# Kernel tuning notes

Hardware: AMD Instinct MI355X
Metric: run time of the kernel (lower is better)

The kernel has to match this reference:

```python
import jax, jax.numpy as jnp
import numpy as np

B, S, D, H, F = 8, 1024, 1024, 16, 4096
DH = D // H  # 64
EPS = 1e-12


def _layer_norm(x, g, b):
    mu = jnp.mean(x, axis=-1, keepdims=True)
    var = jnp.mean(jnp.square(x - mu), axis=-1, keepdims=True)
    return (x - mu) / jnp.sqrt(var + EPS) * g + b


def setup_inputs() -> dict:
    key = jax.random.key(0)
    ks = jax.random.split(key, 16)
    sd = 0.02
    inp = {
        "x": jax.random.normal(ks[0], (B, S, D), dtype=jnp.float32),
        "attn_mask": jnp.ones((B, S), dtype=jnp.int32),
        # attention projections (torch Linear: W is [out, in])
        "Wq": jax.random.normal(ks[1], (D, D), dtype=jnp.float32) * sd,
        "bq": jnp.zeros((D,), dtype=jnp.float32),
        "Wk": jax.random.normal(ks[2], (D, D), dtype=jnp.float32) * sd,
        "bk": jnp.zeros((D,), dtype=jnp.float32),
        "Wv": jax.random.normal(ks[3], (D, D), dtype=jnp.float32) * sd,
        "bv": jnp.zeros((D,), dtype=jnp.float32),
        "Wo": jax.random.normal(ks[4], (D, D), dtype=jnp.float32) * sd,
        "bo": jnp.zeros((D,), dtype=jnp.float32),
        # sa_layer_norm
        "ln1_g": jnp.ones((D,), dtype=jnp.float32),
        "ln1_b": jnp.zeros((D,), dtype=jnp.float32),
        # FFN
        "W1": jax.random.normal(ks[5], (F, D), dtype=jnp.float32) * sd,
        "b1": jnp.zeros((F,), dtype=jnp.float32),
        "W2": jax.random.normal(ks[6], (D, F), dtype=jnp.float32) * sd,
        "b2": jnp.zeros((D,), dtype=jnp.float32),
        # output_layer_norm
        "ln2_g": jnp.ones((D,), dtype=jnp.float32),
        "ln2_b": jnp.zeros((D,), dtype=jnp.float32),
    }
    return inp


def reference(x, attn_mask, Wq, bq, Wk, bk, Wv, bv, Wo, bo,
              ln1_g, ln1_b, W1, b1, W2, b2, ln2_g, ln2_b):
    b, s, d = x.shape

    def proj_heads(inp, W, bias):
        y = jnp.einsum('bsd,ed->bse', inp, W) + bias  # torch Linear: x @ W.T + b
        return y.reshape(b, s, H, DH).transpose(0, 2, 1, 3)  # (b, h, s, dh)

    q = proj_heads(x, Wq, bq) / jnp.sqrt(jnp.float32(DH))
    k = proj_heads(x, Wk, bk)
    v = proj_heads(x, Wv, bv)

    scores = jnp.einsum('bhqe,bhke->bhqk', q, k)  # (b, h, s, s)
    pad = (attn_mask == 0)[:, None, None, :]      # (b, 1, 1, s)
    scores = jnp.where(pad, -jnp.inf, scores)
    weights = jax.nn.softmax(scores, axis=-1)

    ctx = jnp.einsum('bhqk,bhke->bhqe', weights, v)
    ctx = ctx.transpose(0, 2, 1, 3).reshape(b, s, d)
    sa_out = jnp.einsum('bsd,ed->bse', ctx, Wo) + bo

    h = _layer_norm(sa_out + x, ln1_g, ln1_b)

    ff = jnp.einsum('bsd,fd->bsf', h, W1) + b1
    ff = jax.nn.gelu(ff, approximate=False)
    ff = jnp.einsum('bsf,df->bsd', ff, W2) + b2

    out = _layer_norm(ff + h, ln2_g, ln2_b)
    return out
```

## Files before the change

### kernel.cpp

```cpp
#include <hip/hip_runtime.h>
#include <math.h>

typedef __attribute__((ext_vector_type(8))) short short8;
typedef __attribute__((ext_vector_type(4))) float f32x4;

__device__ __forceinline__ unsigned short f2bf(float f) {
  unsigned int u = __float_as_uint(f);
  u += 0x7fffu + ((u >> 16) & 1u);
  return (unsigned short)(u >> 16);
}

__device__ __forceinline__ float gelu_f(float v) {
  float xa = fabsf(v) * 0.70710678118f;
  float t = __builtin_amdgcn_rcpf(1.f + 0.3275911f * xa);
  float p = t * (0.254829592f +
            t * (-0.284496736f +
            t * (1.421413741f +
            t * (-1.453152027f + t * 1.061405429f))));
  float erfa = 1.f - p * __expf(-xa * xa);
  return 0.5f * v * (1.f + copysignf(erfa, v));
}

__device__ __forceinline__ void gll16(const unsigned short* g, unsigned short* l) {
  __builtin_amdgcn_global_load_lds(
      (const __attribute__((address_space(1))) unsigned int*)(uintptr_t)g,
      (__attribute__((address_space(3))) unsigned int*)(uintptr_t)l, 16, 0, 0);
}

__global__ __launch_bounds__(256) void cvt_all(
    const float* __restrict__ Wq, const float* __restrict__ Wk,
    const float* __restrict__ Wv, const float* __restrict__ Wo,
    const float* __restrict__ W1, const float* __restrict__ W2,
    const float* __restrict__ x, unsigned short* __restrict__ ws) {
  const int bi = blockIdx.x;
  const float* in;
  unsigned short* out;
  int i;
  if (bi < 4096) {
    const int m = bi >> 10;
    in = (m == 0) ? Wq : (m == 1) ? Wk : (m == 2) ? Wv : Wo;
    out = ws + (size_t)m * (1u << 20);
    i = (bi & 1023) * 256 + threadIdx.x;
  } else if (bi < 8192) {
    in = W1; out = ws + (4u << 20); i = (bi - 4096) * 256 + threadIdx.x;
  } else if (bi < 12288) {
    in = W2; out = ws + (8u << 20); i = (bi - 8192) * 256 + threadIdx.x;
  } else {
    in = x; out = ws + (12u << 20); i = (bi - 12288) * 256 + threadIdx.x;
  }
  float4 f = reinterpret_cast<const float4*>(in)[i];
  ushort4 o;
  o.x = f2bf(f.x); o.y = f2bf(f.y); o.z = f2bf(f.z); o.w = f2bf(f.w);
  reinterpret_cast<ushort4*>(out)[i] = o;
}

#define MFMA_SUB(f0, SA)                                                      \
  {                                                                           \
    __builtin_amdgcn_s_setprio(1);                                            \
    _Pragma("unroll") for (int fi = 0; fi < 2; ++fi) {                        \
      _Pragma("unroll") for (int j = 0; j < NREP; ++j) {                      \
        if constexpr (SWAP) {                                                 \
          acc[(f0) + fi][j] = __builtin_amdgcn_mfma_f32_16x16x32_bf16(        \
              bf[j][0], SA[fi][0], acc[(f0) + fi][j], 0, 0, 0);               \
        } else {                                                              \
          acc[(f0) + fi][j] = __builtin_amdgcn_mfma_f32_16x16x32_bf16(        \
              SA[fi][0], bf[j][0], acc[(f0) + fi][j], 0, 0, 0);               \
        }                                                                     \
      }                                                                       \
    }                                                                         \
    _Pragma("unroll") for (int fi = 0; fi < 2; ++fi) {                        \
      _Pragma("unroll") for (int j = 0; j < NREP; ++j) {                      \
        if constexpr (SWAP) {                                                 \
          acc[(f0) + fi][j] = __builtin_amdgcn_mfma_f32_16x16x32_bf16(        \
              bf[j][1], SA[fi][1], acc[(f0) + fi][j], 0, 0, 0);               \
        } else {                                                              \
          acc[(f0) + fi][j] = __builtin_amdgcn_mfma_f32_16x16x32_bf16(        \
              SA[fi][1], bf[j][1], acc[(f0) + fi][j], 0, 0, 0);               \
        }                                                                     \
      }                                                                       \
    }                                                                         \
    __builtin_amdgcn_s_setprio(0);                                            \
  }

#define READ_AF(SET, f0)                                                      \
  {                                                                           \
    SET[0][0] = *reinterpret_cast<const short8*>(                             \
        &Asc[abase + ((f0) * 16) * 64 + s0]);                                 \
    SET[0][1] = *reinterpret_cast<const short8*>(                             \
        &Asc[abase + ((f0) * 16) * 64 + s1]);                                 \
    SET[1][0] = *reinterpret_cast<const short8*>(                             \
        &Asc[abase + ((f0) * 16 + 16) * 64 + s0]);                            \
    SET[1][1] = *reinterpret_cast<const short8*>(                             \
        &Asc[abase + ((f0) * 16 + 16) * 64 + s1]);                            \
  }

#define READ_BF                                                               \
  _Pragma("unroll") for (int j = 0; j < NREP; ++j) {                          \
    bf[j][0] = *reinterpret_cast<const short8*>(                              \
        &Bsc[bbase + (j * 16) * 64 + s0]);                                    \
    bf[j][1] = *reinterpret_cast<const short8*>(                              \
        &Bsc[bbase + (j * 16) * 64 + s1]);                                    \
  }

#define LGKM(n)                                                               \
  asm volatile("s_waitcnt lgkmcnt(" #n ")" ::: "memory");                     \
  __builtin_amdgcn_sched_barrier(0)

#define MEMFENCE asm volatile("" ::: "memory")
#define BAR __builtin_amdgcn_s_barrier()

template <int EPI, int BN, bool SWAP>
__global__ __launch_bounds__(512, 2) void gemm_big(
    const unsigned short* __restrict__ A, const unsigned short* __restrict__ B,
    const float* __restrict__ bias, const float* __restrict__ bias_k,
    int K, int N, const float* __restrict__ resid,
    unsigned short* __restrict__ outb, float* __restrict__ outf) {
  constexpr int WN = BN / 4;
  constexpr int NREP = WN / 16;
  constexpr int BGRP = BN / 64;
  __shared__ __align__(16) unsigned short As[2][256 * 64];
  __shared__ __align__(16) unsigned short Bs[2][BN * 64];

  const int t = threadIdx.x;
  const int lane = t & 63, wv = t >> 6;
  const int wm = wv >> 2, wn = wv & 3;
  const int l15 = lane & 15, quad = lane >> 4;

  const int gx = gridDim.x;
  const int nwg = gx * gridDim.y;
  int lin = blockIdx.y * gx + blockIdx.x;
  lin = (lin & 7) * (nwg >> 3) + (lin >> 3);
  const int gxs = 31 - __clz(gx);
  const int tn = (lin & (gx - 1)) * BN;
  const int tm = (lin >> gxs) * 256;

  const int srow = lane >> 3;
  const int scol = ((lane & 7) ^ srow) << 3;
  const unsigned short* pA[4];
  const unsigned short* pB[BGRP];
#pragma unroll
  for (int g = 0; g < 4; ++g)
    pA[g] = &A[(size_t)(tm + g * 64 + wv * 8 + srow) * K + scol];
#pragma unroll
  for (int g = 0; g < BGRP; ++g)
    pB[g] = &B[(size_t)(tn + g * 64 + wv * 8 + srow) * K + scol];

  const int abase = (wm * 128 + l15) * 64;
  const int bbase = (wn * WN + l15) * 64;
  const int s0 = ((quad ^ (l15 & 7)) << 3);
  const int s1 = (((quad + 4) ^ (l15 & 7)) << 3);

  const f32x4 zero = {0.f, 0.f, 0.f, 0.f};
  f32x4 acc[8][NREP];
#pragma unroll
  for (int i = 0; i < 8; ++i)
#pragma unroll
    for (int j = 0; j < NREP; ++j) acc[i][j] = zero;
  short8 afA[2][2], afB[2][2], bf[NREP][2];

#pragma unroll
  for (int g = 0; g < 4; ++g) {
    gll16(pA[g], &As[0][(g * 64 + wv * 8) * 64]);
    pA[g] += 64;
  }
#pragma unroll
  for (int g = 0; g < BGRP; ++g) {
    gll16(pB[g], &Bs[0][(g * 64 + wv * 8) * 64]);
    pB[g] += 64;
  }
  asm volatile("s_waitcnt vmcnt(0)" ::: "memory");
  BAR;
  MEMFENCE;

  const int NT = K >> 6;
  for (int tt = 0; tt < NT; ++tt) {
    const unsigned short* Asc = As[tt & 1];
    const unsigned short* Bsc = Bs[tt & 1];
    unsigned short* Asn = As[(tt + 1) & 1];
    unsigned short* Bsn = Bs[(tt + 1) & 1];

    if (tt + 1 < NT) {
#pragma unroll
      for (int g = 0; g < 4; ++g) {
        gll16(pA[g], &Asn[(g * 64 + wv * 8) * 64]);
        pA[g] += 64;
      }
#pragma unroll
      for (int g = 0; g < BGRP; ++g) {
        gll16(pB[g], &Bsn[(g * 64 + wv * 8) * 64]);
        pB[g] += 64;
      }
    }

    READ_BF;
    READ_AF(afA, 0);
    READ_AF(afB, 2);
    LGKM(4);
    MFMA_SUB(0, afA);
    READ_AF(afA, 4);
    LGKM(4);
    MFMA_SUB(2, afB);
    READ_AF(afB, 6);
    LGKM(4);
    MFMA_SUB(4, afA);
    LGKM(0);
    MFMA_SUB(6, afB);

    if (tt + 1 < NT) {
      asm volatile("s_waitcnt vmcnt(0)" ::: "memory");
      BAR;
      MEMFENCE;
    }
  }

  if constexpr (!SWAP) {
    const int rb2 = tm + wm * 128 + (quad << 2);
    const int cb2 = tn + wn * WN + l15;
#pragma unroll
    for (int i = 0; i < 8; ++i) {
      const int row0 = rb2 + i * 16;
#pragma unroll
      for (int j = 0; j < NREP; ++j) {
        const int col = cb2 + j * 16;
        const float bcol = bias[col];
        const int h = col >> 6, dh = col & 63;
        const int b = row0 >> 10, s0r = row0 & 1023;
        ushort4 pk;
        pk.x = f2bf(acc[i][j][0] + bcol);
        pk.y = f2bf(acc[i][j][1] + bcol);
        pk.z = f2bf(acc[i][j][2] + bcol);
        pk.w = f2bf(acc[i][j][3] + bcol);
        *reinterpret_cast<ushort4*>(
            &outb[(((size_t)((b << 4) + h)) << 16) + (dh << 10) + s0r]) = pk;
      }
    }
  } else {
    const int rb = tm + wm * 128 + l15;
    const int cb = tn + wn * WN + (quad << 2);
#pragma unroll
    for (int i = 0; i < 8; ++i) {
      const int row = rb + i * 16;
#pragma unroll
      for (int j = 0; j < NREP; ++j) {
        const int col0 = cb + j * 16;
        if constexpr (EPI == 5) {
          const int chunk = col0 >> 10;
          const int colc = col0 & 1023;
          const float4 b4 = *reinterpret_cast<const float4*>(
              &(chunk == 0 ? bias : bias_k)[colc]);
          const float sc = (chunk == 0) ? 0.125f : 1.f;
          const int h = colc >> 6, dh = colc & 63;
          const int b = row >> 10, s = row & 1023;
          ushort4 pk;
          pk.x = f2bf((acc[i][j][0] + b4.x) * sc);
          pk.y = f2bf((acc[i][j][1] + b4.y) * sc);
          pk.z = f2bf((acc[i][j][2] + b4.z) * sc);
          pk.w = f2bf((acc[i][j][3] + b4.w) * sc);
          *reinterpret_cast<ushort4*>(
              &outb[((size_t)chunk << 23) + (((size_t)((b << 4) + h)) << 16) +
                    (s << 6) + dh]) = pk;
        } else if constexpr (EPI == 2) {
          const float4 b4 = *reinterpret_cast<const float4*>(&bias[col0]);
          ushort4 pk;
          pk.x = f2bf(gelu_f(acc[i][j][0] + b4.x));
          pk.y = f2bf(gelu_f(acc[i][j][1] + b4.y));
          pk.z = f2bf(gelu_f(acc[i][j][2] + b4.z));
          pk.w = f2bf(gelu_f(acc[i][j][3] + b4.w));
          *reinterpret_cast<ushort4*>(&outb[(size_t)row * (size_t)N + col0]) = pk;
        } else {
          const float4 b4 = *reinterpret_cast<const float4*>(&bias[col0]);
          const size_t idx = (size_t)row * (size_t)N + col0;
          const float4 r4 = *reinterpret_cast<const float4*>(&resid[idx]);
          float4 o4;
          o4.x = acc[i][j][0] + b4.x + r4.x;
          o4.y = acc[i][j][1] + b4.y + r4.y;
          o4.z = acc[i][j][2] + b4.z + r4.z;
          o4.w = acc[i][j][3] + b4.w + r4.w;
          *reinterpret_cast<float4*>(&outf[idx]) = o4;
        }
      }
    }
  }
}
#undef MFMA_SUB
#undef READ_AF
#undef READ_BF
#undef LGKM
#undef MEMFENCE
#undef BAR

__global__ __launch_bounds__(256) void attn_kernel(
    const unsigned short* __restrict__ Q, const unsigned short* __restrict__ Kc,
    const unsigned short* __restrict__ Vg, const int* __restrict__ mask,
    unsigned short* __restrict__ ctx) {
  __shared__ __align__(16) unsigned short Ks[2][64 * 64];
  __shared__ __align__(16) unsigned short Vs[2][64 * 64];
  __shared__ __align__(16) unsigned short Ps[4][16 * 72];
  __shared__ float maskf[1024];
  const int t = threadIdx.x;
  const int bh = blockIdx.x;
  const int qt = blockIdx.y;
  const int b = bh >> 4, h = bh & 15;
  const int lane = t & 63, wv = t >> 6, l15 = lane & 15, quad = lane >> 4;
  const int lr = lane >> 3;
  const int cs = (lane & 7) ^ lr;
  const unsigned short* Qp = Q + ((size_t)bh << 16);
  const unsigned short* Kp = Kc + ((size_t)bh << 16);
  const unsigned short* Vp = Vg + ((size_t)bh << 16);
  const int seg0 = wv * 2, seg1 = wv * 2 + 1;
  const int r0 = seg0 * 8 + lr, r1 = seg1 * 8 + lr;

  for (int i = t; i < 1024; i += 256)
    maskf[i] = mask[b * 1024 + i] ? -8.f : -INFINITY;

  short8 qf[2][2];
#pragma unroll
  for (int g = 0; g < 2; ++g)
#pragma unroll
    for (int hh = 0; hh < 2; ++hh)
      qf[g][hh] = *reinterpret_cast<const short8*>(
          &Qp[(size_t)(qt * 128 + wv * 32 + g * 16 + l15) * 64 + hh * 32 + quad * 8]);

  gll16(&Kp[r0 * 64 + cs * 8], &Ks[0][seg0 * 512]);
  gll16(&Kp[r1 * 64 + cs * 8], &Ks[0][seg1 * 512]);
  gll16(&Vp[r0 * 1024 + cs * 8], &Vs[0][seg0 * 512]);
  gll16(&Vp[r1 * 1024 + cs * 8], &Vs[0][seg1 * 512]);

  const int sw0 = ((quad ^ (l15 & 7)) << 3);
  const int sw1 = (((quad + 4) ^ (l15 & 7)) << 3);
  const f32x4 zero = {0.f, 0.f, 0.f, 0.f};
  float ps[2][4];
  f32x4 o[2][4];
#pragma unroll
  for (int g = 0; g < 2; ++g)
#pragma unroll
    for (int j = 0; j < 4; ++j) { o[g][j] = zero; ps[g][j] = 0.f; }

  unsigned short* Pw = Ps[wv];
  for (int kt = 0; kt < 16; ++kt) {
    __syncthreads();
    const int cur = kt & 1;
    if (kt < 15) {
      const int nb = cur ^ 1;
      gll16(&Kp[((kt + 1) * 64 + r0) * 64 + cs * 8], &Ks[nb][seg0 * 512]);
      gll16(&Kp[((kt + 1) * 64 + r1) * 64 + cs * 8], &Ks[nb][seg1 * 512]);
      gll16(&Vp[r0 * 1024 + (kt + 1) * 64 + cs * 8], &Vs[nb][seg0 * 512]);
      gll16(&Vp[r1 * 1024 + (kt + 1) * 64 + cs * 8], &Vs[nb][seg1 * 512]);
    }
    float madd[4];
    short8 kf[4][2];
#pragma unroll
    for (int nt = 0; nt < 4; ++nt) {
      const int row = (nt * 16 + l15) * 64;
      kf[nt][0] = *reinterpret_cast<const short8*>(&Ks[cur][row + sw0]);
      kf[nt][1] = *reinterpret_cast<const short8*>(&Ks[cur][row + sw1]);
      madd[nt] = maskf[kt * 64 + nt * 16 + l15];
    }
#pragma unroll
    for (int g = 0; g < 2; ++g) {
      f32x4 s4[4];
#pragma unroll
      for (int nt = 0; nt < 4; ++nt)
        s4[nt] = __builtin_amdgcn_mfma_f32_16x16x32_bf16(qf[g][0], kf[nt][0], zero, 0, 0, 0);
#pragma unroll
      for (int nt = 0; nt < 4; ++nt)
        s4[nt] = __builtin_amdgcn_mfma_f32_16x16x32_bf16(qf[g][1], kf[nt][1], s4[nt], 0, 0, 0);
#pragma unroll
      for (int nt = 0; nt < 4; ++nt) {
#pragma unroll
        for (int r = 0; r < 4; ++r) {
          float p = __expf(s4[nt][r] + madd[nt]);
          ps[g][r] += p;
          Pw[(quad * 4 + r) * 72 + nt * 16 + l15] = f2bf(p);
        }
      }
      short8 pf0 = *reinterpret_cast<const short8*>(&Pw[l15 * 72 + quad * 8]);
      short8 pf1 = *reinterpret_cast<const short8*>(&Pw[l15 * 72 + 32 + quad * 8]);
      short8 vf[4][2];
#pragma unroll
      for (int nt = 0; nt < 4; ++nt) {
        const int row = (nt * 16 + l15) * 64;
        vf[nt][0] = *reinterpret_cast<const short8*>(&Vs[cur][row + sw0]);
        vf[nt][1] = *reinterpret_cast<const short8*>(&Vs[cur][row + sw1]);
      }
#pragma unroll
      for (int nt = 0; nt < 4; ++nt)
        o[g][nt] = __builtin_amdgcn_mfma_f32_16x16x32_bf16(pf0, vf[nt][0], o[g][nt], 0, 0, 0);
#pragma unroll
      for (int nt = 0; nt < 4; ++nt)
        o[g][nt] = __builtin_amdgcn_mfma_f32_16x16x32_bf16(pf1, vf[nt][1], o[g][nt], 0, 0, 0);
    }
  }

#pragma unroll
  for (int g = 0; g < 2; ++g)
#pragma unroll
    for (int r = 0; r < 4; ++r) {
      float v = ps[g][r];
#pragma unroll
      for (int off = 8; off >= 1; off >>= 1) v += __shfl_xor(v, off, 64);
      const float inv = 1.f / v;
      const int srow = qt * 128 + wv * 32 + g * 16 + quad * 4 + r;
#pragma unroll
      for (int nt = 0; nt < 4; ++nt) {
        const int dh = nt * 16 + l15;
        ctx[((size_t)b << 20) + ((size_t)srow << 10) + (h << 6) + dh] =
            f2bf(o[g][nt][r] * inv);
      }
    }
}

__global__ __launch_bounds__(256) void ln_kernel(float* __restrict__ y,
                                                 const float* __restrict__ g,
                                                 const float* __restrict__ be,
                                                 unsigned short* __restrict__ hb) {
  __shared__ float sm[8];
  const int t = threadIdx.x;
  const size_t row = blockIdx.x;
  float* yr = y + (row << 10);
  float v[4];
#pragma unroll
  for (int i = 0; i < 4; ++i) v[i] = yr[t + (i << 8)];
  float s = v[0] + v[1] + v[2] + v[3];
#pragma unroll
  for (int off = 32; off >= 1; off >>= 1) s += __shfl_xor(s, off, 64);
  if ((t & 63) == 0) sm[t >> 6] = s;
  __syncthreads();
  float mu = (sm[0] + sm[1] + sm[2] + sm[3]) * (1.f / 1024.f);
  float q = 0.f;
#pragma unroll
  for (int i = 0; i < 4; ++i) { float d = v[i] - mu; q += d * d; }
#pragma unroll
  for (int off = 32; off >= 1; off >>= 1) q += __shfl_xor(q, off, 64);
  if ((t & 63) == 0) sm[4 + (t >> 6)] = q;
  __syncthreads();
  float var = (sm[4] + sm[5] + sm[6] + sm[7]) * (1.f / 1024.f);
  float rs = rsqrtf(var + 1e-12f);
#pragma unroll
  for (int i = 0; i < 4; ++i) {
    int c = t + (i << 8);
    float o = (v[i] - mu) * rs * g[c] + be[c];
    yr[c] = o;
    if (hb) hb[(row << 10) + c] = f2bf(o);
  }
}

extern "C" void kernel_launch(void* const* d_in, const int* in_sizes, int n_in,
                              void* d_out, int out_size, void* d_ws, size_t ws_size,
                              hipStream_t stream) {
  const float* x   = (const float*)d_in[0];
  const int*   msk = (const int*)d_in[1];
  const float* Wq  = (const float*)d_in[2];
  const float* bq  = (const float*)d_in[3];
  const float* Wk  = (const float*)d_in[4];
  const float* bk  = (const float*)d_in[5];
  const float* Wv  = (const float*)d_in[6];
  const float* bv  = (const float*)d_in[7];
  const float* Wo  = (const float*)d_in[8];
  const float* bo  = (const float*)d_in[9];
  const float* g1  = (const float*)d_in[10];
  const float* be1 = (const float*)d_in[11];
  const float* W1  = (const float*)d_in[12];
  const float* b1  = (const float*)d_in[13];
  const float* W2  = (const float*)d_in[14];
  const float* b2  = (const float*)d_in[15];
  const float* g2  = (const float*)d_in[16];
  const float* be2 = (const float*)d_in[17];
  float* out = (float*)d_out;

  unsigned short* Wqb = (unsigned short*)d_ws;
  unsigned short* Wvb = Wqb + (2u << 20);
  unsigned short* Wob = Wvb + (1u << 20);
  unsigned short* W1b = Wob + (1u << 20);
  unsigned short* W2b = W1b + (4u << 20);
  unsigned short* xb  = W2b + (4u << 20);
  unsigned short* qb  = xb + (8u << 20);
  unsigned short* vb  = qb + (16u << 20);
  unsigned short* ctx = xb;
  unsigned short* ffb = xb;
  float* y1 = (float*)(qb + (24u << 20));
  unsigned short* hb = (unsigned short*)(y1 + (8u << 20));

  dim3 blk(256), blk5(512);
  cvt_all<<<dim3(20480), blk, 0, stream>>>(Wq, Wk, Wv, Wo, W1, W2, x, (unsigned short*)d_ws);
  gemm_big<5, 256, true><<<dim3(8, 32), blk5, 0, stream>>>(xb, Wqb, bq, bk, 1024, 2048,
                                                           nullptr, qb, nullptr);
  gemm_big<4, 128, false><<<dim3(8, 32), blk5, 0, stream>>>(xb, Wvb, bv, nullptr, 1024, 1024,
                                                            nullptr, vb, nullptr);
  attn_kernel<<<dim3(128, 8), blk, 0, stream>>>(qb, qb + (8u << 20), vb, msk, ctx);
  gemm_big<1, 128, true><<<dim3(8, 32), blk5, 0, stream>>>(ctx, Wob, bo, nullptr, 1024, 1024,
                                                           x, nullptr, y1);
  ln_kernel<<<dim3(8192), blk, 0, stream>>>(y1, g1, be1, hb);
  gemm_big<2, 256, true><<<dim3(16, 32), blk5, 0, stream>>>(hb, W1b, b1, nullptr, 1024, 4096,
                                                            nullptr, ffb, nullptr);
  gemm_big<1, 128, true><<<dim3(8, 32), blk5, 0, stream>>>(ffb, W2b, b2, nullptr, 4096, 1024,
                                                           y1, nullptr, out);
  ln_kernel<<<dim3(8192), blk, 0, stream>>>(out, g2, be2, nullptr);
}
```

Measured before the change: 485.9 us.

## Load K and V fragments directly from global memory in attention kernel

Removes the double-buffered LDS staging of K and V tiles, along with the per-iteration barrier, and has each wave read its MFMA K and V fragments straight from global memory into registers. The aim is to cut LDS traffic, synchronisation and LDS footprint, which could raise occupancy. In exchange every wave loads the same K/V data redundantly through the cache hierarchy, and the global loads are no longer overlapped with compute by explicit prefetching, so latency may be exposed.

```diff
diff --git a/kernel.cpp b/kernel.cpp
--- a/kernel.cpp
+++ b/kernel.cpp
@@ -293,8 +293,6 @@
     const unsigned short* __restrict__ Q, const unsigned short* __restrict__ Kc,
     const unsigned short* __restrict__ Vg, const int* __restrict__ mask,
     unsigned short* __restrict__ ctx) {
-  __shared__ __align__(16) unsigned short Ks[2][64 * 64];
-  __shared__ __align__(16) unsigned short Vs[2][64 * 64];
   __shared__ __align__(16) unsigned short Ps[4][16 * 72];
   __shared__ float maskf[1024];
   const int t = threadIdx.x;
@@ -302,13 +300,9 @@
   const int qt = blockIdx.y;
   const int b = bh >> 4, h = bh & 15;
   const int lane = t & 63, wv = t >> 6, l15 = lane & 15, quad = lane >> 4;
-  const int lr = lane >> 3;
-  const int cs = (lane & 7) ^ lr;
   const unsigned short* Qp = Q + ((size_t)bh << 16);
   const unsigned short* Kp = Kc + ((size_t)bh << 16);
   const unsigned short* Vp = Vg + ((size_t)bh << 16);
-  const int seg0 = wv * 2, seg1 = wv * 2 + 1;
-  const int r0 = seg0 * 8 + lr, r1 = seg1 * 8 + lr;
 
   for (int i = t; i < 1024; i += 256)
     maskf[i] = mask[b * 1024 + i] ? -8.f : -INFINITY;
@@ -321,13 +315,6 @@
       qf[g][hh] = *reinterpret_cast<const short8*>(
           &Qp[(size_t)(qt * 128 + wv * 32 + g * 16 + l15) * 64 + hh * 32 + quad * 8]);
 
-  gll16(&Kp[r0 * 64 + cs * 8], &Ks[0][seg0 * 512]);
-  gll16(&Kp[r1 * 64 + cs * 8], &Ks[0][seg1 * 512]);
-  gll16(&Vp[r0 * 1024 + cs * 8], &Vs[0][seg0 * 512]);
-  gll16(&Vp[r1 * 1024 + cs * 8], &Vs[0][seg1 * 512]);
-
-  const int sw0 = ((quad ^ (l15 & 7)) << 3);
-  const int sw1 = (((quad + 4) ^ (l15 & 7)) << 3);
   const f32x4 zero = {0.f, 0.f, 0.f, 0.f};
   float ps[2][4];
   f32x4 o[2][4];
@@ -336,25 +323,25 @@
 #pragma unroll
     for (int j = 0; j < 4; ++j) { o[g][j] = zero; ps[g][j] = 0.f; }
 
+  __syncthreads();
+
   unsigned short* Pw = Ps[wv];
   for (int kt = 0; kt < 16; ++kt) {
-    __syncthreads();
-    const int cur = kt & 1;
-    if (kt < 15) {
-      const int nb = cur ^ 1;
-      gll16(&Kp[((kt + 1) * 64 + r0) * 64 + cs * 8], &Ks[nb][seg0 * 512]);
-      gll16(&Kp[((kt + 1) * 64 + r1) * 64 + cs * 8], &Ks[nb][seg1 * 512]);
-      gll16(&Vp[r0 * 1024 + (kt + 1) * 64 + cs * 8], &Vs[nb][seg0 * 512]);
-      gll16(&Vp[r1 * 1024 + (kt + 1) * 64 + cs * 8], &Vs[nb][seg1 * 512]);
-    }
     float madd[4];
     short8 kf[4][2];
 #pragma unroll
     for (int nt = 0; nt < 4; ++nt) {
-      const int row = (nt * 16 + l15) * 64;
-      kf[nt][0] = *reinterpret_cast<const short8*>(&Ks[cur][row + sw0]);
-      kf[nt][1] = *reinterpret_cast<const short8*>(&Ks[cur][row + sw1]);
+      const int krow = kt * 64 + nt * 16 + l15;
+      kf[nt][0] = *reinterpret_cast<const short8*>(&Kp[(size_t)krow * 64 + quad * 8]);
+      kf[nt][1] = *reinterpret_cast<const short8*>(&Kp[(size_t)krow * 64 + 32 + quad * 8]);
       madd[nt] = maskf[kt * 64 + nt * 16 + l15];
+    }
+    short8 vf[4][2];
+#pragma unroll
+    for (int nt = 0; nt < 4; ++nt) {
+      const int dh = nt * 16 + l15;
+      vf[nt][0] = *reinterpret_cast<const short8*>(&Vp[(size_t)dh * 1024 + kt * 64 + quad * 8]);
+      vf[nt][1] = *reinterpret_cast<const short8*>(&Vp[(size_t)dh * 1024 + kt * 64 + 32 + quad * 8]);
     }
 #pragma unroll
     for (int g = 0; g < 2; ++g) {
@@ -376,13 +363,6 @@
       }
       short8 pf0 = *reinterpret_cast<const short8*>(&Pw[l15 * 72 + quad * 8]);
       short8 pf1 = *reinterpret_cast<const short8*>(&Pw[l15 * 72 + 32 + quad * 8]);
-      short8 vf[4][2];
-#pragma unroll
-      for (int nt = 0; nt < 4; ++nt) {
-        const int row = (nt * 16 + l15) * 64;
-        vf[nt][0] = *reinterpret_cast<const short8*>(&Vs[cur][row + sw0]);
-        vf[nt][1] = *reinterpret_cast<const short8*>(&Vs[cur][row + sw1]);
-      }
 #pragma unroll
       for (int nt = 0; nt < 4; ++nt)
         o[g][nt] = __builtin_amdgcn_mfma_f32_16x16x32_bf16(pf0, vf[nt][0], o[g][nt], 0, 0, 0);
```

Measured after the change: 531.5 us. 9.4% more time.
